# Performance work log

Measured on AMD Instinct MI355X. Metric: run time of the kernel, lower is better.

The kernel has to match this reference:

```python
import jax, jax.numpy as jnp
import numpy as np
import math

B = 8192
LAT, COND, OUT = 64, 256, 512
HID, E, NLAYER, GH = 1024, 8, 3, 128
INPUT = LAT + COND          # 320
INTER = LAT + HID           # 1088
EPS = 1e-5


def _ln(x):
    # F.layer_norm(input, input.shape[1:]) -> no affine, eps=1e-5, over last dim
    m = jnp.mean(x, axis=-1, keepdims=True)
    v = jnp.var(x, axis=-1, keepdims=True)
    return (x - m) * jax.lax.rsqrt(v + EPS)


def setup_inputs() -> dict:
    key = jax.random.key(0)
    ks = jax.random.split(key, 24)
    d = {}
    d['z'] = jax.random.normal(ks[0], (B, LAT), jnp.float32)
    d['c'] = jax.random.normal(ks[1], (B, COND), jnp.float32)
    # gate MLP params (PyTorch Linear default init scale ~ 1/sqrt(fan_in))
    gate_dims = [(INPUT, GH), (GH, GH), (GH, E)]
    for i, (fi, fo) in enumerate(gate_dims):
        s = 1.0 / math.sqrt(fi)
        d[f'g{i}_w'] = jax.random.uniform(ks[2 + 2 * i], (fi, fo), jnp.float32, -s, s)
        d[f'g{i}_b'] = jax.random.uniform(ks[3 + 2 * i], (fo,), jnp.float32, -s, s)
    # expert decoder layers: weight [E, in, out], bias [E, out], stdv = 1/sqrt(in)
    for i in range(NLAYER + 1):
        fi = INPUT if i == 0 else INTER
        fo = HID if i != NLAYER else OUT
        s = 1.0 / math.sqrt(fi)
        d[f'w{i}'] = jax.random.uniform(ks[8 + 2 * i], (E, fi, fo), jnp.float32, -s, s)
        d[f'b{i}'] = jax.random.uniform(ks[9 + 2 * i], (E, fo), jnp.float32, -s, s)
    return d


def reference(z, c, g0_w, g0_b, g1_w, g1_b, g2_w, g2_b,
              w0, b0, w1, b1, w2, b2, w3, b3):
    x = jnp.concatenate([z, c], axis=-1)                    # [B, INPUT]
    h = jax.nn.elu(x @ g0_w + g0_b)
    h = jax.nn.elu(h @ g1_w + g1_b)
    coeff = jax.nn.softmax(h @ g2_w + g2_b, axis=-1)        # [B, E]

    layer_out = c
    layers = [(w0, b0, True), (w1, b1, True), (w2, b2, True), (w3, b3, False)]
    for w, b, act in layers:
        inp = _ln(jnp.concatenate([z, layer_out], axis=-1))  # [B, J]
        per = jnp.einsum('bj,ejk->ebk', inp, w)              # per-expert outputs
        out = jnp.einsum('be,ebk->bk', coeff, per) + coeff @ b
        layer_out = jax.nn.elu(out) if act else out
    return layer_out
```

## Files before the change

### kernel.cpp

```cpp
#include <hip/hip_runtime.h>
#include <cstdint>
#include <cstddef>

#define B_ROWS 8192
#define E_EXP  8

typedef unsigned short ushort_t;
typedef short bf16x8 __attribute__((ext_vector_type(8)));
typedef float f32x4  __attribute__((ext_vector_type(4)));
typedef float f32x16 __attribute__((ext_vector_type(16)));

__device__ __forceinline__ ushort_t f2b(float f) {
  union { float f; unsigned int i; } v; v.f = f;
  unsigned int u = v.i;
  unsigned int r = (u + 0x7fffu + ((u >> 16) & 1u)) >> 16;
  return (ushort_t)r;
}
__device__ __forceinline__ float eluf(float x) {
  return x > 0.f ? x : (__expf(x) - 1.f);
}

__global__ void transpose_k(const float* __restrict__ src,
                            ushort_t* __restrict__ dst, int R, int C) {
  __shared__ ushort_t tile[64][65];
  int c0 = blockIdx.x * 64, r0 = blockIdx.y * 64;
  int x = threadIdx.x, y = threadIdx.y;
#pragma unroll
  for (int i = 0; i < 4; ++i)
    tile[y + 16 * i][x] = f2b(src[(size_t)(r0 + y + 16 * i) * C + c0 + x]);
  __syncthreads();
#pragma unroll
  for (int i = 0; i < 4; ++i)
    dst[(size_t)(c0 + y + 16 * i) * R + r0 + x] = tile[x][y + 16 * i];
}

__global__ __launch_bounds__(128) void gate_k(
    const float* __restrict__ z, const float* __restrict__ c,
    const float* __restrict__ g0w, const float* __restrict__ g0b,
    const float* __restrict__ g1w, const float* __restrict__ g1b,
    const float* __restrict__ g2w, const float* __restrict__ g2b,
    float* __restrict__ coeff, float* __restrict__ rat2,
    float* __restrict__ rat4) {
  __shared__ float xs[4][320];
  __shared__ float h1[4][128];
  __shared__ float h2[4][128];
  __shared__ float lg[4][8];
  __shared__ float pr[4][8];
  int t = threadIdx.x;
  int r0 = blockIdx.x * 4;
  for (int idx = t; idx < 4 * 320; idx += 128) {
    int r = idx / 320, j = idx % 320;
    xs[r][j] = (j < 64) ? z[(size_t)(r0 + r) * 64 + j]
                        : c[(size_t)(r0 + r) * 256 + j - 64];
  }
  __syncthreads();
  {
    float bb = g0b[t];
    float a0 = bb, a1 = bb, a2 = bb, a3 = bb;
    for (int j = 0; j < 320; j += 4) {
      float w0 = g0w[j * 128 + t];
      float w1 = g0w[(j + 1) * 128 + t];
      float w2 = g0w[(j + 2) * 128 + t];
      float w3 = g0w[(j + 3) * 128 + t];
      float4 x0 = *(const float4*)&xs[0][j];
      float4 x1 = *(const float4*)&xs[1][j];
      float4 x2 = *(const float4*)&xs[2][j];
      float4 x3 = *(const float4*)&xs[3][j];
      a0 += x0.x * w0 + x0.y * w1 + x0.z * w2 + x0.w * w3;
      a1 += x1.x * w0 + x1.y * w1 + x1.z * w2 + x1.w * w3;
      a2 += x2.x * w0 + x2.y * w1 + x2.z * w2 + x2.w * w3;
      a3 += x3.x * w0 + x3.y * w1 + x3.z * w2 + x3.w * w3;
    }
    h1[0][t] = eluf(a0); h1[1][t] = eluf(a1);
    h1[2][t] = eluf(a2); h1[3][t] = eluf(a3);
  }
  __syncthreads();
  {
    float bb = g1b[t];
    float a0 = bb, a1 = bb, a2 = bb, a3 = bb;
    for (int j = 0; j < 128; j += 4) {
      float w0 = g1w[j * 128 + t];
      float w1 = g1w[(j + 1) * 128 + t];
      float w2 = g1w[(j + 2) * 128 + t];
      float w3 = g1w[(j + 3) * 128 + t];
      float4 x0 = *(const float4*)&h1[0][j];
      float4 x1 = *(const float4*)&h1[1][j];
      float4 x2 = *(const float4*)&h1[2][j];
      float4 x3 = *(const float4*)&h1[3][j];
      a0 += x0.x * w0 + x0.y * w1 + x0.z * w2 + x0.w * w3;
      a1 += x1.x * w0 + x1.y * w1 + x1.z * w2 + x1.w * w3;
      a2 += x2.x * w0 + x2.y * w1 + x2.z * w2 + x2.w * w3;
      a3 += x3.x * w0 + x3.y * w1 + x3.z * w2 + x3.w * w3;
    }
    h2[0][t] = eluf(a0); h2[1][t] = eluf(a1);
    h2[2][t] = eluf(a2); h2[3][t] = eluf(a3);
  }
  __syncthreads();
  if (t < 32) {
    int r = t >> 3, e = t & 7;
    float a = g2b[e];
    for (int j = 0; j < 128; ++j) a += h2[r][j] * g2w[j * 8 + e];
    lg[r][e] = a;
  }
  __syncthreads();
  if (t < 32) {
    int r = t >> 3, e = t & 7;
    float mx = lg[r][0];
#pragma unroll
    for (int i = 1; i < 8; ++i) mx = fmaxf(mx, lg[r][i]);
    float s = 0.f;
#pragma unroll
    for (int i = 0; i < 8; ++i) s += __expf(lg[r][i] - mx);
    float p = __expf(lg[r][e] - mx) / s;
    coeff[(size_t)(r0 + r) * 8 + e] = p;
    pr[r][e] = p;
  }
  __syncthreads();
  if (t < 32) {
    int r = t >> 3, e = t & 7;
    float pe = pr[r][e];
    float ratio = (e < 7) ? pe / fmaxf(pr[r][e + 1], 1e-30f) : pe;
    rat2[(size_t)(r0 + r) * 8 + e] = (e == 3 || e == 7) ? pe : ratio;
    rat4[(size_t)(r0 + r) * 8 + e] = (e & 1) ? pe : ratio;
  }
}

__global__ __launch_bounds__(128) void ln_concat_k(
    const float* __restrict__ z, const float* __restrict__ p0,
    const float* __restrict__ p1, const float* __restrict__ cf,
    const float* __restrict__ bias, ushort_t* __restrict__ out,
    int Pw, int J) {
  int row = blockIdx.x, t = threadIdx.x;
  float vals[9];
  int n = (J + 127) >> 7;
  float cr[8];
  if (p1) {
#pragma unroll
    for (int e = 0; e < 8; ++e) cr[e] = cf[(size_t)row * 8 + e];
  }
  float s = 0.f, s2 = 0.f;
  for (int k = 0; k < n; ++k) {
    int i = t + (k << 7);
    float x = 0.f;
    if (i < J) {
      if (i < 64) {
        x = z[(size_t)row * 64 + i];
      } else if (p1) {
        int j = i - 64;
        float v = p0[(size_t)row * Pw + j] + p1[(size_t)row * Pw + j];
#pragma unroll
        for (int e = 0; e < 8; ++e) v += cr[e] * bias[(size_t)e * Pw + j];
        x = eluf(v);
      } else {
        x = p0[(size_t)row * Pw + i - 64];
      }
    }
    vals[k] = x; s += x; s2 += x * x;
  }
  for (int off = 32; off > 0; off >>= 1) {
    s += __shfl_down(s, off);
    s2 += __shfl_down(s2, off);
  }
  __shared__ float red[4];
  int wid = t >> 6, lane = t & 63;
  if (lane == 0) { red[wid * 2] = s; red[wid * 2 + 1] = s2; }
  __syncthreads();
  float S = red[0] + red[2], S2 = red[1] + red[3];
  float inv = 1.f / (float)J;
  float m = S * inv;
  float var = S2 * inv - m * m;
  float rstd = rsqrtf(var + 1e-5f);
  for (int k = 0; k < n; ++k) {
    int i = t + (k << 7);
    if (i < J) out[(size_t)row * J + i] = f2b((vals[k] - m) * rstd);
  }
}

__device__ __forceinline__ void gload16(const void* g, void* l) {
  __builtin_amdgcn_global_load_lds(
      (const __attribute__((address_space(1))) void*)g,
      (__attribute__((address_space(3))) void*)l, 16, 0, 0);
}

__global__ __launch_bounds__(512, 2) void moe_gemm_k(
    const ushort_t* __restrict__ inp,
    const ushort_t* __restrict__ wT,
    const float* __restrict__ scales,
    float* __restrict__ outp,
    int J, int K, int ne) {
  const int Kd = E_EXP * J;
  const int nj = J >> 6;
  const int nt = ne * nj;
  __shared__ short As[2][2][16 * 512];
  __shared__ short Wsm[2][2][16 * 512];
  __shared__ float scale_s[256 * 9];

  const int t = threadIdx.x;
  const int w = t >> 6, l = t & 63;
  const int wm = w >> 2, wn = w & 3;
  const int lr  = l & 31;
  const int lh  = (l & 31) >> 4;
  const int lk  = l >> 5;
  const int lro = (l & 15) * 8;
  const int bt = blockIdx.x, ct = blockIdx.y, ez = blockIdx.z;
  const int e0 = ez * ne;
  outp += (size_t)ez * (size_t)B_ROWS * (size_t)K;

#pragma unroll
  for (int i = 0; i < 4; ++i) {
    int idx = t + (i << 9);
    int rw = idx >> 3, e = idx & 7;
    scale_s[rw * 9 + e] = scales[(size_t)(bt * 256 + rw) * 8 + e];
  }

  size_t abase[2], wbase[2];
#pragma unroll
  for (int i = 0; i < 2; ++i) {
    int g = w * 2 + i;
    abase[i] = (size_t)(bt * 256 + g * 16 + (l & 15)) * J + ((l >> 4) * 8);
    wbase[i] = (size_t)(ct * 256 + g * 16 + (l & 15)) * Kd + (size_t)e0 * J +
               ((l >> 4) * 8);
  }
  int s_acol = 0, s_wcol = 0, sjt = 0;

  auto stageA = [&](int nb, int ks) {
    short* d = &As[nb][ks][w * 2 * 512];
    gload16(inp + abase[0] + s_acol + ks * 32, d);
    gload16(inp + abase[1] + s_acol + ks * 32, d + 512);
  };
  auto stageW = [&](int nb, int ks) {
    short* d = &Wsm[nb][ks][w * 2 * 512];
    gload16(wT + wbase[0] + s_wcol + ks * 32, d);
    gload16(wT + wbase[1] + s_wcol + ks * 32, d + 512);
  };
  auto advance = [&]() {
    s_wcol += 64;
    if (++sjt == nj) { sjt = 0; s_acol = 0; } else { s_acol += 64; }
  };

  f32x16 acc[4][2];
#pragma unroll
  for (int R = 0; R < 4; ++R)
#pragma unroll
    for (int C = 0; C < 2; ++C)
#pragma unroll
      for (int q = 0; q < 16; ++q) acc[R][C][q] = 0.f;

  auto rdA = [&](bf16x8* dst, const short* half, int s) {
#pragma unroll
    for (int R = 0; R < 4; ++R)
      dst[R] = *(const bf16x8*)(half + (wm * 8 + R * 2 + lh) * 512 + lro +
                                (s * 2 + lk) * 128);
  };
  auto rdW = [&](bf16x8(*dst)[2], const short* half) {
#pragma unroll
    for (int s = 0; s < 2; ++s)
#pragma unroll
      for (int C = 0; C < 2; ++C)
        dst[s][C] = *(const bf16x8*)(half + (wn * 4 + C * 2 + lh) * 512 + lro +
                                     (s * 2 + lk) * 128);
  };

#define MM8(AF, BF)                                                        \
  __builtin_amdgcn_s_setprio(1);                                           \
  _Pragma("unroll") for (int R = 0; R < 4; ++R)                            \
      _Pragma("unroll") for (int C = 0; C < 2; ++C) acc[R][C] =            \
          __builtin_amdgcn_mfma_f32_32x32x16_bf16(AF[R], BF[C],            \
                                                  acc[R][C], 0, 0, 0);     \
  __builtin_amdgcn_s_setprio(0);

  stageA(0, 0); stageW(0, 0); stageA(0, 1); stageW(0, 1); advance();
  __syncthreads();

  int cjt = 0, cle = 0;
  for (int tp = 0; tp < nt; ++tp) {
    const int b = tp & 1, nb = b ^ 1;
    const bool more = (tp + 1 < nt);
    const short* A0 = &As[b][0][0];
    const short* A1 = &As[b][1][0];
    const short* W0 = &Wsm[b][0][0];
    const short* W1 = &Wsm[b][1][0];
    bf16x8 af[4], bf[2][2];

    if (more) stageA(nb, 0);
    rdW(bf, W0);
    rdA(af, A0, 0);
    MM8(af, bf[0]);
    if (more) stageW(nb, 0);
    rdA(af, A0, 1);
    MM8(af, bf[1]);
    if (more) asm volatile("s_waitcnt vmcnt(4)" ::: "memory");
    else      asm volatile("s_waitcnt vmcnt(0)" ::: "memory");
    asm volatile("s_barrier" ::: "memory");
    if (more) stageA(nb, 1);
    rdW(bf, W1);
    rdA(af, A1, 0);
    MM8(af, bf[0]);
    if (more) { stageW(nb, 1); advance(); }
    rdA(af, A1, 1);
    MM8(af, bf[1]);
    if (++cjt == nj) {
      cjt = 0;
      int e = e0 + cle;
      ++cle;
#pragma unroll
      for (int R = 0; R < 4; ++R) {
#pragma unroll
        for (int q = 0; q < 16; ++q) {
          int row = wm * 128 + R * 32 + (q & 3) + 8 * (q >> 2) + 4 * lk;
          float rv = scale_s[row * 9 + e];
          acc[R][0][q] *= rv;
          acc[R][1][q] *= rv;
        }
      }
    }
    if (more) asm volatile("s_waitcnt vmcnt(4)" ::: "memory");
    else      asm volatile("s_waitcnt vmcnt(0)" ::: "memory");
    asm volatile("s_barrier" ::: "memory");
  }

#pragma unroll
  for (int R = 0; R < 4; ++R) {
#pragma unroll
    for (int q = 0; q < 16; ++q) {
      int row = wm * 128 + R * 32 + (q & 3) + 8 * (q >> 2) + 4 * lk;
      size_t orow = (size_t)(bt * 256 + row) * K + ct * 256;
#pragma unroll
      for (int C = 0; C < 2; ++C)
        outp[orow + wn * 64 + C * 32 + lr] = acc[R][C][q];
    }
  }
}

__global__ __launch_bounds__(256) void combine4_k(
    const float* __restrict__ pb, const float* __restrict__ cf,
    const float* __restrict__ bias, float* __restrict__ out, int K) {
  size_t i4 = (size_t)blockIdx.x * 256 + threadIdx.x;
  size_t total = (size_t)B_ROWS * (size_t)K;
  size_t base = i4 * 4;
  if (base >= total) return;
  int row = (int)(base / (size_t)K);
  int col = (int)(base % (size_t)K);
  size_t s4 = total >> 2;
  const f32x4* p4 = (const f32x4*)pb;
  f32x4 v = p4[i4] + p4[i4 + s4] + p4[i4 + 2 * s4] + p4[i4 + 3 * s4];
#pragma unroll
  for (int e = 0; e < 8; ++e) {
    float ce = cf[(size_t)row * 8 + e];
    f32x4 bv = *(const f32x4*)(bias + (size_t)e * K + col);
    v += ce * bv;
  }
  ((f32x4*)out)[i4] = v;
}

extern "C" void kernel_launch(void* const* d_in, const int* in_sizes, int n_in,
                              void* d_out, int out_size, void* d_ws, size_t ws_size,
                              hipStream_t stream) {
  const float* z   = (const float*)d_in[0];
  const float* c   = (const float*)d_in[1];
  const float* g0w = (const float*)d_in[2];
  const float* g0b = (const float*)d_in[3];
  const float* g1w = (const float*)d_in[4];
  const float* g1b = (const float*)d_in[5];
  const float* g2w = (const float*)d_in[6];
  const float* g2b = (const float*)d_in[7];
  const float* w0  = (const float*)d_in[8];
  const float* b0  = (const float*)d_in[9];
  const float* w1  = (const float*)d_in[10];
  const float* b1  = (const float*)d_in[11];
  const float* w2  = (const float*)d_in[12];
  const float* b2  = (const float*)d_in[13];
  const float* w3  = (const float*)d_in[14];
  const float* b3  = (const float*)d_in[15];

  char* ws = (char*)d_ws;
  size_t o = 0;
  auto alloc = [&](size_t bytes) {
    void* p = ws + o;
    o += (bytes + 255) & ~(size_t)255;
    return p;
  };
  ushort_t* wT0 = (ushort_t*)alloc((size_t)2560 * 1024 * 2);
  ushort_t* wT1 = (ushort_t*)alloc((size_t)8704 * 1024 * 2);
  ushort_t* wT2 = (ushort_t*)alloc((size_t)8704 * 1024 * 2);
  ushort_t* wT3 = (ushort_t*)alloc((size_t)8704 * 512 * 2);
  float*    cf   = (float*)alloc((size_t)B_ROWS * 8 * 4);
  float*    rat2 = (float*)alloc((size_t)B_ROWS * 8 * 4);
  float*    rat4 = (float*)alloc((size_t)B_ROWS * 8 * 4);
  ushort_t* inp  = (ushort_t*)alloc((size_t)B_ROWS * 1088 * 2);
  float*    pb   = (float*)alloc((size_t)2 * B_ROWS * 1024 * 4);

  dim3 tb(64, 16);
  transpose_k<<<dim3(1024 / 64, 2560 / 64), tb, 0, stream>>>(w0, wT0, 2560, 1024);
  transpose_k<<<dim3(1024 / 64, 8704 / 64), tb, 0, stream>>>(w1, wT1, 8704, 1024);
  transpose_k<<<dim3(1024 / 64, 8704 / 64), tb, 0, stream>>>(w2, wT2, 8704, 1024);
  transpose_k<<<dim3(512 / 64, 8704 / 64), tb, 0, stream>>>(w3, wT3, 8704, 512);

  gate_k<<<B_ROWS / 4, 128, 0, stream>>>(z, c, g0w, g0b, g1w, g1b, g2w, g2b,
                                         cf, rat2, rat4);

  float* p1v = pb + (size_t)B_ROWS * 1024;

  ln_concat_k<<<B_ROWS, 128, 0, stream>>>(z, c, nullptr, nullptr, nullptr,
                                          inp, 256, 320);
  moe_gemm_k<<<dim3(32, 4, 2), 512, 0, stream>>>(inp, wT0, rat2, pb, 320, 1024, 4);
  ln_concat_k<<<B_ROWS, 128, 0, stream>>>(z, pb, p1v, cf, b0, inp, 1024, 1088);
  moe_gemm_k<<<dim3(32, 4, 2), 512, 0, stream>>>(inp, wT1, rat2, pb, 1088, 1024, 4);
  ln_concat_k<<<B_ROWS, 128, 0, stream>>>(z, pb, p1v, cf, b1, inp, 1024, 1088);
  moe_gemm_k<<<dim3(32, 4, 2), 512, 0, stream>>>(inp, wT2, rat2, pb, 1088, 1024, 4);
  ln_concat_k<<<B_ROWS, 128, 0, stream>>>(z, pb, p1v, cf, b2, inp, 1024, 1088);
  moe_gemm_k<<<dim3(32, 2, 4), 512, 0, stream>>>(inp, wT3, rat4, pb, 1088, 512, 2);
  combine4_k<<<(B_ROWS * 512) / 1024, 256, 0, stream>>>(pb, cf, b3,
                                                        (float*)d_out, 512);
}
```

Before: 740.6 us.

## Switch MoE GEMM to 1024-thread blocks with 16x16x32 MFMA tiles

The MoE GEMM now runs 16 waves per block instead of 8. Each wave computes a 64x64 sub-tile using 16x16x32 bf16 MFMAs with f32x4 accumulators, replacing 128x64 tiles built from 32x32x16 MFMAs. Each thread issues one async global-to-LDS load per stage instead of two, and the waitcnt thresholds and epilogue index maps are adjusted to match. The aim is more waves to hide latency and less register pressure per wave. The cost is more LDS fragment reads per FLOP, the lower throughput of the smaller MFMA shape, and only one block per CU.

```diff
diff --git a/kernel.cpp b/kernel.cpp
--- a/kernel.cpp
+++ b/kernel.cpp
@@ -8,7 +8,6 @@
 typedef unsigned short ushort_t;
 typedef short bf16x8 __attribute__((ext_vector_type(8)));
 typedef float f32x4  __attribute__((ext_vector_type(4)));
-typedef float f32x16 __attribute__((ext_vector_type(16)));
 
 __device__ __forceinline__ ushort_t f2b(float f) {
   union { float f; unsigned int i; } v; v.f = f;
@@ -182,7 +181,7 @@
       (__attribute__((address_space(3))) void*)l, 16, 0, 0);
 }
 
-__global__ __launch_bounds__(512, 2) void moe_gemm_k(
+__global__ __launch_bounds__(1024, 1) void moe_gemm_k(
     const ushort_t* __restrict__ inp,
     const ushort_t* __restrict__ wT,
     const float* __restrict__ scales,
@@ -198,75 +197,55 @@
   const int t = threadIdx.x;
   const int w = t >> 6, l = t & 63;
   const int wm = w >> 2, wn = w & 3;
-  const int lr  = l & 31;
-  const int lh  = (l & 31) >> 4;
-  const int lk  = l >> 5;
-  const int lro = (l & 15) * 8;
   const int bt = blockIdx.x, ct = blockIdx.y, ez = blockIdx.z;
   const int e0 = ez * ne;
   outp += (size_t)ez * (size_t)B_ROWS * (size_t)K;
 
 #pragma unroll
-  for (int i = 0; i < 4; ++i) {
-    int idx = t + (i << 9);
+  for (int i = 0; i < 2; ++i) {
+    int idx = t + (i << 10);
     int rw = idx >> 3, e = idx & 7;
     scale_s[rw * 9 + e] = scales[(size_t)(bt * 256 + rw) * 8 + e];
   }
 
-  size_t abase[2], wbase[2];
-#pragma unroll
-  for (int i = 0; i < 2; ++i) {
-    int g = w * 2 + i;
-    abase[i] = (size_t)(bt * 256 + g * 16 + (l & 15)) * J + ((l >> 4) * 8);
-    wbase[i] = (size_t)(ct * 256 + g * 16 + (l & 15)) * Kd + (size_t)e0 * J +
-               ((l >> 4) * 8);
-  }
+  size_t abase = (size_t)(bt * 256 + w * 16 + (l & 15)) * J + ((l >> 4) * 8);
+  size_t wbase = (size_t)(ct * 256 + w * 16 + (l & 15)) * Kd +
+                 (size_t)e0 * J + ((l >> 4) * 8);
   int s_acol = 0, s_wcol = 0, sjt = 0;
 
   auto stageA = [&](int nb, int ks) {
-    short* d = &As[nb][ks][w * 2 * 512];
-    gload16(inp + abase[0] + s_acol + ks * 32, d);
-    gload16(inp + abase[1] + s_acol + ks * 32, d + 512);
+    gload16(inp + abase + s_acol + ks * 32, &As[nb][ks][w * 512]);
   };
   auto stageW = [&](int nb, int ks) {
-    short* d = &Wsm[nb][ks][w * 2 * 512];
-    gload16(wT + wbase[0] + s_wcol + ks * 32, d);
-    gload16(wT + wbase[1] + s_wcol + ks * 32, d + 512);
+    gload16(wT + wbase + s_wcol + ks * 32, &Wsm[nb][ks][w * 512]);
   };
   auto advance = [&]() {
     s_wcol += 64;
     if (++sjt == nj) { sjt = 0; s_acol = 0; } else { s_acol += 64; }
   };
 
-  f32x16 acc[4][2];
-#pragma unroll
-  for (int R = 0; R < 4; ++R)
-#pragma unroll
-    for (int C = 0; C < 2; ++C)
-#pragma unroll
-      for (int q = 0; q < 16; ++q) acc[R][C][q] = 0.f;
-
-  auto rdA = [&](bf16x8* dst, const short* half, int s) {
-#pragma unroll
-    for (int R = 0; R < 4; ++R)
-      dst[R] = *(const bf16x8*)(half + (wm * 8 + R * 2 + lh) * 512 + lro +
-                                (s * 2 + lk) * 128);
-  };
-  auto rdW = [&](bf16x8(*dst)[2], const short* half) {
-#pragma unroll
-    for (int s = 0; s < 2; ++s)
-#pragma unroll
-      for (int C = 0; C < 2; ++C)
-        dst[s][C] = *(const bf16x8*)(half + (wn * 4 + C * 2 + lh) * 512 + lro +
-                                     (s * 2 + lk) * 128);
-  };
-
-#define MM8(AF, BF)                                                        \
+  f32x4 acc[4][4];
+#pragma unroll
+  for (int q = 0; q < 4; ++q)
+#pragma unroll
+    for (int fn = 0; fn < 4; ++fn) acc[q][fn] = (f32x4){0.f, 0.f, 0.f, 0.f};
+
+#define RDB(ks_)                                                           \
+  _Pragma("unroll") for (int fn = 0; fn < 4; ++fn) bf[fn] =                \
+      *(const bf16x8*)(&Wsm[b][ks_][(wn * 4 + fn) * 512 + l * 8]);
+
+#define RDA2(d0, d1, ks_, q0)                                              \
+  d0 = *(const bf16x8*)(&As[b][ks_][(wm * 4 + (q0)) * 512 + l * 8]);       \
+  d1 = *(const bf16x8*)(&As[b][ks_][(wm * 4 + (q0) + 1) * 512 + l * 8]);
+
+#define MM2(q0, a0_, a1_)                                                  \
   __builtin_amdgcn_s_setprio(1);                                           \
-  _Pragma("unroll") for (int R = 0; R < 4; ++R)                            \
-      _Pragma("unroll") for (int C = 0; C < 2; ++C) acc[R][C] =            \
-          __builtin_amdgcn_mfma_f32_32x32x16_bf16(AF[R], BF[C],            \
-                                                  acc[R][C], 0, 0, 0);     \
+  _Pragma("unroll") for (int fn = 0; fn < 4; ++fn) {                       \
+    acc[(q0)][fn] = __builtin_amdgcn_mfma_f32_16x16x32_bf16(               \
+        a0_, bf[fn], acc[(q0)][fn], 0, 0, 0);                              \
+    acc[(q0) + 1][fn] = __builtin_amdgcn_mfma_f32_16x16x32_bf16(           \
+        a1_, bf[fn], acc[(q0) + 1][fn], 0, 0, 0);                          \
+  }                                                                        \
   __builtin_amdgcn_s_setprio(0);
 
   stageA(0, 0); stageW(0, 0); stageA(0, 1); stageW(0, 1); advance();
@@ -276,58 +255,56 @@
   for (int tp = 0; tp < nt; ++tp) {
     const int b = tp & 1, nb = b ^ 1;
     const bool more = (tp + 1 < nt);
-    const short* A0 = &As[b][0][0];
-    const short* A1 = &As[b][1][0];
-    const short* W0 = &Wsm[b][0][0];
-    const short* W1 = &Wsm[b][1][0];
-    bf16x8 af[4], bf[2][2];
+    bf16x8 bf[4], a0, a1;
 
     if (more) stageA(nb, 0);
-    rdW(bf, W0);
-    rdA(af, A0, 0);
-    MM8(af, bf[0]);
+    RDB(0);
+    RDA2(a0, a1, 0, 0);
+    MM2(0, a0, a1);
     if (more) stageW(nb, 0);
-    rdA(af, A0, 1);
-    MM8(af, bf[1]);
-    if (more) asm volatile("s_waitcnt vmcnt(4)" ::: "memory");
+    RDA2(a0, a1, 0, 2);
+    MM2(2, a0, a1);
+    if (more) asm volatile("s_waitcnt vmcnt(2)" ::: "memory");
     else      asm volatile("s_waitcnt vmcnt(0)" ::: "memory");
     asm volatile("s_barrier" ::: "memory");
     if (more) stageA(nb, 1);
-    rdW(bf, W1);
-    rdA(af, A1, 0);
-    MM8(af, bf[0]);
+    RDB(1);
+    RDA2(a0, a1, 1, 0);
+    MM2(0, a0, a1);
     if (more) { stageW(nb, 1); advance(); }
-    rdA(af, A1, 1);
-    MM8(af, bf[1]);
+    RDA2(a0, a1, 1, 2);
+    MM2(2, a0, a1);
     if (++cjt == nj) {
       cjt = 0;
       int e = e0 + cle;
       ++cle;
 #pragma unroll
-      for (int R = 0; R < 4; ++R) {
-#pragma unroll
-        for (int q = 0; q < 16; ++q) {
-          int row = wm * 128 + R * 32 + (q & 3) + 8 * (q >> 2) + 4 * lk;
-          float rv = scale_s[row * 9 + e];
-          acc[R][0][q] *= rv;
-          acc[R][1][q] *= rv;
+      for (int q = 0; q < 4; ++q) {
+        int rbase = wm * 64 + q * 16 + ((l >> 4) << 2);
+#pragma unroll
+        for (int rr = 0; rr < 4; ++rr) {
+          float rv = scale_s[(rbase + rr) * 9 + e];
+#pragma unroll
+          for (int fn = 0; fn < 4; ++fn) acc[q][fn][rr] *= rv;
         }
       }
     }
-    if (more) asm volatile("s_waitcnt vmcnt(4)" ::: "memory");
+    if (more) asm volatile("s_waitcnt vmcnt(2)" ::: "memory");
     else      asm volatile("s_waitcnt vmcnt(0)" ::: "memory");
     asm volatile("s_barrier" ::: "memory");
   }
 
 #pragma unroll
-  for (int R = 0; R < 4; ++R) {
-#pragma unroll
-    for (int q = 0; q < 16; ++q) {
-      int row = wm * 128 + R * 32 + (q & 3) + 8 * (q >> 2) + 4 * lk;
+  for (int q = 0; q < 4; ++q) {
+#pragma unroll
+    for (int rr = 0; rr < 4; ++rr) {
+      int row = wm * 64 + q * 16 + ((l >> 4) << 2) + rr;
       size_t orow = (size_t)(bt * 256 + row) * K + ct * 256;
 #pragma unroll
-      for (int C = 0; C < 2; ++C)
-        outp[orow + wn * 64 + C * 32 + lr] = acc[R][C][q];
+      for (int fn = 0; fn < 4; ++fn) {
+        int col = wn * 64 + fn * 16 + (l & 15);
+        outp[orow + col] = acc[q][fn][rr];
+      }
     }
   }
 }
@@ -403,13 +380,13 @@
 
   ln_concat_k<<<B_ROWS, 128, 0, stream>>>(z, c, nullptr, nullptr, nullptr,
                                           inp, 256, 320);
-  moe_gemm_k<<<dim3(32, 4, 2), 512, 0, stream>>>(inp, wT0, rat2, pb, 320, 1024, 4);
+  moe_gemm_k<<<dim3(32, 4, 2), 1024, 0, stream>>>(inp, wT0, rat2, pb, 320, 1024, 4);
   ln_concat_k<<<B_ROWS, 128, 0, stream>>>(z, pb, p1v, cf, b0, inp, 1024, 1088);
-  moe_gemm_k<<<dim3(32, 4, 2), 512, 0, stream>>>(inp, wT1, rat2, pb, 1088, 1024, 4);
+  moe_gemm_k<<<dim3(32, 4, 2), 1024, 0, stream>>>(inp, wT1, rat2, pb, 1088, 1024, 4);
   ln_concat_k<<<B_ROWS, 128, 0, stream>>>(z, pb, p1v, cf, b1, inp, 1024, 1088);
-  moe_gemm_k<<<dim3(32, 4, 2), 512, 0, stream>>>(inp, wT2, rat2, pb, 1088, 1024, 4);
+  moe_gemm_k<<<dim3(32, 4, 2), 1024, 0, stream>>>(inp, wT2, rat2, pb, 1088, 1024, 4);
   ln_concat_k<<<B_ROWS, 128, 0, stream>>>(z, pb, p1v, cf, b2, inp, 1024, 1088);
-  moe_gemm_k<<<dim3(32, 2, 4), 512, 0, stream>>>(inp, wT3, rat4, pb, 1088, 512, 2);
+  moe_gemm_k<<<dim3(32, 2, 4), 1024, 0, stream>>>(inp, wT3, rat4, pb, 1088, 512, 2);
   combine4_k<<<(B_ROWS * 512) / 1024, 256, 0, stream>>>(pb, cf, b3,
                                                         (float*)d_out, 512);
 }
```

Measured after the change: 693.1 us. -6.4%, faster.
